# Performance work log

Hardware: AMD Instinct MI355X
Metric: run time of the kernel (lower is better)

Reference implementation:

```python
import jax, jax.numpy as jnp
import numpy as np

DECAY_FACTOR = 0.995
TEMPERATURE = 0.1
MIN_SIMILARITY = 0.0
EPS = 1e-8

B, N, D, H, F, K = 1024, 100000, 512, 96, 7, 16


def setup_inputs() -> dict:
    key = jax.random.key(0)
    k1, k2, k3, k4 = jax.random.split(key, 4)
    query = jax.random.normal(k1, (B, D), dtype=jnp.float32)
    keys = jax.random.normal(k2, (N, D), dtype=jnp.float32)
    values = jax.random.normal(k3, (N, H, F), dtype=jnp.float32)
    timestamps = jnp.sort(jax.random.randint(k4, (N,), 0, 5000).astype(jnp.int64))
    return {
        "query": query,
        "keys": keys,
        "values": values,
        "timestamps": timestamps,
        "global_step": 5000,
        "top_k": K,
    }


def _l2_normalize(x, axis=-1):
    # matches F.normalize(p=2): x / max(||x||, eps) -- use eps in denom
    norm = jnp.sqrt(jnp.sum(x * x, axis=axis, keepdims=True))
    return x / jnp.maximum(norm, 1e-12)


def reference(query, keys, values, timestamps, global_step, top_k):
    # cosine similarity between queries and all memory keys: [B, N]
    q_n = _l2_normalize(query)
    k_n = _l2_normalize(keys)
    sims = jnp.einsum("bd,nd->bn", q_n, k_n)

    # temporal decay by entry age
    age = (global_step - timestamps).astype(jnp.float32)  # [N]
    decay = jnp.power(jnp.float32(DECAY_FACTOR), age)
    sims = sims * decay[None, :]

    # top-k retrieval
    top_sims, top_idx = jax.lax.top_k(sims, top_k)  # [B, K]
    retrieved = values[top_idx]  # [B, K, H, F]

    valid_mask = top_sims >= MIN_SIMILARITY  # [B, K]

    # temperature-weighted aggregation of retrieved error patterns
    weights = jax.nn.softmax(top_sims / TEMPERATURE, axis=-1)
    weights = weights * valid_mask.astype(weights.dtype)
    weights = weights / (jnp.sum(weights, axis=-1, keepdims=True) + EPS)
    corrected = jnp.einsum("bk,bkhf->bhf", weights, retrieved)  # [B, H, F]
    return corrected
```

## Files before the change

### kernel.cpp

```cpp
#include <hip/hip_runtime.h>
#include <math.h>

#define B 1024
#define N 100000
#define D 512
#define H 96
#define F 7
#define K 16
#define HF (H*F)

#define QT 128
#define KT 128
#define NKT 784
#define NPAD (NKT*KT)

#define GQ 32
#define NG (NPAD/GQ)
#define SELG 16
#define CAND (SELG*GQ)
#define CSEL 32

typedef __attribute__((ext_vector_type(8))) short shortx8;
typedef __attribute__((ext_vector_type(4))) float floatx4;

__device__ __forceinline__ unsigned short f2bf(float f) {
    unsigned int u = __float_as_uint(f);
    u += 0x7FFF + ((u >> 16) & 1);
    return (unsigned short)(u >> 16);
}
__device__ __forceinline__ float bf2f(unsigned short u) {
    return __uint_as_float((unsigned)u << 16);
}

#define ASYNC16(g, l) __builtin_amdgcn_global_load_lds( \
    (__attribute__((address_space(1))) void*)(g), \
    (__attribute__((address_space(3))) void*)(l), 16, 0, 0)

__global__ void prep_q(const float* __restrict__ q, float* __restrict__ qn,
                       unsigned short* __restrict__ qb) {
    int w = (blockIdx.x * blockDim.x + threadIdx.x) >> 6;
    int l = threadIdx.x & 63;
    if (w >= B) return;
    const float4* row = (const float4*)(q + (size_t)w * D);
    float4 a = row[l], b = row[l + 64];
    float ss = a.x*a.x + a.y*a.y + a.z*a.z + a.w*a.w
             + b.x*b.x + b.y*b.y + b.z*b.z + b.w*b.w;
#pragma unroll
    for (int off = 32; off; off >>= 1) ss += __shfl_xor(ss, off);
    float nrm = fmaxf(sqrtf(ss), 1e-12f);
    a.x /= nrm; a.y /= nrm; a.z /= nrm; a.w /= nrm;
    b.x /= nrm; b.y /= nrm; b.z /= nrm; b.w /= nrm;
    float4* o = (float4*)(qn + (size_t)w * D);
    o[l] = a; o[l + 64] = b;
    unsigned short* ob = qb + (size_t)w * D;
    *(ushort4*)(ob + 4*l)       = make_ushort4(f2bf(a.x), f2bf(a.y), f2bf(a.z), f2bf(a.w));
    *(ushort4*)(ob + 256 + 4*l) = make_ushort4(f2bf(b.x), f2bf(b.y), f2bf(b.z), f2bf(b.w));
}

__global__ void prep_k(const float* __restrict__ keys, const int* __restrict__ ts,
                       const int* __restrict__ gstep, float* __restrict__ kscale,
                       unsigned short* __restrict__ kb) {
    int w = (blockIdx.x * blockDim.x + threadIdx.x) >> 6;
    int l = threadIdx.x & 63;
    if (w >= NPAD) return;
    unsigned short* dst = kb + (size_t)w * D;
    if (w >= N) {
        *(ushort4*)(dst + 4*l)       = make_ushort4(0,0,0,0);
        *(ushort4*)(dst + 256 + 4*l) = make_ushort4(0,0,0,0);
        return;
    }
    const float4* row = (const float4*)(keys + (size_t)w * D);
    float4 a = row[l], b = row[l + 64];
    float ss = a.x*a.x + a.y*a.y + a.z*a.z + a.w*a.w
             + b.x*b.x + b.y*b.y + b.z*b.z + b.w*b.w;
#pragma unroll
    for (int off = 32; off; off >>= 1) ss += __shfl_xor(ss, off);
    float age = (float)(gstep[0] - ts[w]);
    float sc = powf(0.995f, age) / fmaxf(sqrtf(ss), 1e-12f);
    if (l == 0) kscale[w] = sc;
    *(ushort4*)(dst + 4*l)       = make_ushort4(f2bf(a.x*sc), f2bf(a.y*sc), f2bf(a.z*sc), f2bf(a.w*sc));
    *(ushort4*)(dst + 256 + 4*l) = make_ushort4(f2bf(b.x*sc), f2bf(b.y*sc), f2bf(b.z*sc), f2bf(b.w*sc));
}

__global__ __launch_bounds__(256, 3)
void gmax_k(const unsigned short* __restrict__ qb, const unsigned short* __restrict__ kb,
            float* __restrict__ gmax) {
    __shared__ __align__(16) unsigned short As[QT * 32];
    __shared__ __align__(16) unsigned short Bs[KT * 32];

    const int t = threadIdx.x;
    const int w = t >> 6, l = t & 63;
    const int qbase = blockIdx.x * QT;
    const int kbase = blockIdx.y * KT;
    const int m = l & 15, quad = l >> 4;
    const int wq = w & 1, wk = w >> 1;

    const int srow = l >> 2;
    const int scol = (l & 3) * 8;
    const unsigned short* gA0 = qb + (size_t)(qbase + w*32 + srow) * D + scol;
    const unsigned short* gA1 = gA0 + (size_t)16 * D;
    const unsigned short* gB0 = kb + (size_t)(kbase + w*32 + srow) * D + scol;
    const unsigned short* gB1 = gB0 + (size_t)16 * D;
    unsigned short* lA0 = As + (w*32) * 32;
    unsigned short* lA1 = As + (w*32 + 16) * 32;
    unsigned short* lB0 = Bs + (w*32) * 32;
    unsigned short* lB1 = Bs + (w*32 + 16) * 32;

    const unsigned short* aBase = As + (size_t)(wq*64 + m) * 32 + quad*8;
    const unsigned short* bBase = Bs + (size_t)(wk*64 + m) * 32 + quad*8;

    floatx4 acc[4][4];
#pragma unroll
    for (int i = 0; i < 4; ++i)
#pragma unroll
        for (int j = 0; j < 4; ++j) acc[i][j] = (floatx4){0.f, 0.f, 0.f, 0.f};

    for (int ds = 0; ds < D/32; ++ds) {
        ASYNC16(gA0 + ds*32, lA0);
        ASYNC16(gA1 + ds*32, lA1);
        ASYNC16(gB0 + ds*32, lB0);
        ASYNC16(gB1 + ds*32, lB1);
        __syncthreads();
        shortx8 af[4], bf[4];
#pragma unroll
        for (int i = 0; i < 4; ++i) af[i] = *(const shortx8*)(aBase + i*512);
#pragma unroll
        for (int j = 0; j < 4; ++j) bf[j] = *(const shortx8*)(bBase + j*512);
#pragma unroll
        for (int i = 0; i < 4; ++i)
#pragma unroll
            for (int j = 0; j < 4; ++j)
                acc[i][j] = __builtin_amdgcn_mfma_f32_16x16x32_bf16(
                    af[i], bf[j], acc[i][j], 0, 0, 0);
        __syncthreads();
    }

    const int gcol = blockIdx.y * 4 + wk * 2;
#pragma unroll
    for (int qt = 0; qt < 4; ++qt)
#pragma unroll
        for (int r = 0; r < 4; ++r) {
            float v0 = fmaxf(acc[qt][0][r], acc[qt][1][r]);
            float v1 = fmaxf(acc[qt][2][r], acc[qt][3][r]);
#pragma unroll
            for (int off = 1; off < 16; off <<= 1) {
                v0 = fmaxf(v0, __shfl_xor(v0, off));
                v1 = fmaxf(v1, __shfl_xor(v1, off));
            }
            if (m == 0) {
                size_t row = (size_t)(qbase + wq*64 + qt*16 + quad*4 + r);
                gmax[row * NG + gcol]     = v0;
                gmax[row * NG + gcol + 1] = v1;
            }
        }
}

__global__ __launch_bounds__(256)
void select_out(const float* __restrict__ gmax, const unsigned short* __restrict__ qb,
                const unsigned short* __restrict__ kb, const float* __restrict__ qn,
                const float* __restrict__ keys, const float* __restrict__ kscale,
                const float* __restrict__ values, float* __restrict__ out) {
    int b = blockIdx.x, t = threadIdx.x;
    __shared__ float sG[NG];
    __shared__ int   gSel[SELG];
    __shared__ float eS[CAND];
    __shared__ int   eI[CAND];
    __shared__ float rS[4]; __shared__ int rI[4], rP[4];
    __shared__ float qrow[D];
    __shared__ unsigned short sQ[D];
    __shared__ float cS[CSEL]; __shared__ int cIdx[CSEL];
    __shared__ float wgt[K]; __shared__ int wIdx[K];

    for (int i = t; i < NG; i += 256) sG[i] = gmax[(size_t)b * NG + i];
    for (int i = t; i < D; i += 256) { qrow[i] = qn[(size_t)b * D + i]; sQ[i] = qb[(size_t)b * D + i]; }
    __syncthreads();

    int lane = t & 63, w = t >> 6;

    for (int r = 0; r < SELG; ++r) {
        float best = -INFINITY; int bp = 0x7fffffff;
        for (int i = t; i < NG; i += 256) {
            float v = sG[i];
            if (v > best || (v == best && i < bp)) { best = v; bp = i; }
        }
#pragma unroll
        for (int off = 32; off; off >>= 1) {
            float ob = __shfl_xor(best, off);
            int op = __shfl_xor(bp, off);
            if (ob > best || (ob == best && op < bp)) { best = ob; bp = op; }
        }
        if (lane == 0) { rS[w] = best; rP[w] = bp; }
        __syncthreads();
        if (t == 0) {
            float bb = rS[0]; int bbp = rP[0];
            for (int j = 1; j < 4; ++j)
                if (rS[j] > bb || (rS[j] == bb && rP[j] < bbp)) { bb = rS[j]; bbp = rP[j]; }
            gSel[r] = bbp; sG[bbp] = -INFINITY;
        }
        __syncthreads();
    }

    float qv[8];
#pragma unroll
    for (int j = 0; j < 8; ++j) qv[j] = bf2f(sQ[lane*8 + j]);
    for (int s = w; s < CAND; s += 4) {
        int g = gSel[s >> 5];
        int idx = g * GQ + (s & 31);
        uint4 kv = *(const uint4*)(kb + (size_t)idx * D + lane*8);
        unsigned u0 = kv.x, u1 = kv.y, u2 = kv.z, u3 = kv.w;
        float p = 0.f;
        p = fmaf(qv[0], __uint_as_float((u0 & 0xffffu) << 16), p);
        p = fmaf(qv[1], __uint_as_float(u0 & 0xffff0000u), p);
        p = fmaf(qv[2], __uint_as_float((u1 & 0xffffu) << 16), p);
        p = fmaf(qv[3], __uint_as_float(u1 & 0xffff0000u), p);
        p = fmaf(qv[4], __uint_as_float((u2 & 0xffffu) << 16), p);
        p = fmaf(qv[5], __uint_as_float(u2 & 0xffff0000u), p);
        p = fmaf(qv[6], __uint_as_float((u3 & 0xffffu) << 16), p);
        p = fmaf(qv[7], __uint_as_float(u3 & 0xffff0000u), p);
#pragma unroll
        for (int off = 32; off; off >>= 1) p += __shfl_xor(p, off);
        if (lane == 0) { eS[s] = (idx < N) ? p : -INFINITY; eI[s] = idx; }
    }
    __syncthreads();

    for (int r = 0; r < CSEL; ++r) {
        float best = -INFINITY; int bi = 0x7fffffff, bp = -1;
        for (int i = t; i < CAND; i += 256) {
            float v = eS[i]; int ii = eI[i];
            if (v > best || (v == best && ii < bi)) { best = v; bi = ii; bp = i; }
        }
#pragma unroll
        for (int off = 32; off; off >>= 1) {
            float ob = __shfl_xor(best, off);
            int oi = __shfl_xor(bi, off);
            int op = __shfl_xor(bp, off);
            if (ob > best || (ob == best && oi < bi)) { best = ob; bi = oi; bp = op; }
        }
        if (lane == 0) { rS[w] = best; rI[w] = bi; rP[w] = bp; }
        __syncthreads();
        if (t == 0) {
            float bb = rS[0]; int bbi = rI[0], bbp = rP[0];
            for (int j = 1; j < 4; ++j)
                if (rS[j] > bb || (rS[j] == bb && rI[j] < bbi)) { bb = rS[j]; bbi = rI[j]; bbp = rP[j]; }
            cIdx[r] = bbi;
            if (bbp >= 0) eS[bbp] = -INFINITY;
        }
        __syncthreads();
    }

    for (int c = w; c < CSEL; c += 4) {
        int idx = cIdx[c];
        const float4* kr = (const float4*)(keys + (size_t)idx * D);
        const float4* qr = (const float4*)qrow;
        float4 k1 = kr[lane], k2 = kr[lane + 64];
        float4 q1 = qr[lane], q2 = qr[lane + 64];
        float p = q1.x*k1.x + q1.y*k1.y + q1.z*k1.z + q1.w*k1.w
                + q2.x*k2.x + q2.y*k2.y + q2.z*k2.z + q2.w*k2.w;
#pragma unroll
        for (int off = 32; off; off >>= 1) p += __shfl_xor(p, off);
        if (lane == 0) cS[c] = p * kscale[idx];
    }
    __syncthreads();

    if (t == 0) {
        float s[CSEL]; int id[CSEL];
        for (int i = 0; i < CSEL; ++i) { s[i] = cS[i]; id[i] = cIdx[i]; }
        float selS[K]; int selI[K];
        for (int r = 0; r < K; ++r) {
            float bb = -INFINITY; int bbi = 0x7fffffff, bbp = -1;
            for (int i = 0; i < CSEL; ++i)
                if (s[i] > bb || (s[i] == bb && id[i] < bbi)) { bb = s[i]; bbi = id[i]; bbp = i; }
            selS[r] = bb; selI[r] = bbi; s[bbp] = -INFINITY;
        }
        float y[K], e[K];
        for (int k = 0; k < K; ++k) y[k] = selS[k] / 0.1f;
        float ymax = y[0];
        float Z = 0.f;
        for (int k = 0; k < K; ++k) { e[k] = expf(y[k] - ymax); Z += e[k]; }
        float Z2 = 0.f;
        for (int k = 0; k < K; ++k) {
            float ww = e[k] / Z;
            if (!(selS[k] >= 0.0f)) ww = 0.f;
            e[k] = ww; Z2 += ww;
        }
        for (int k = 0; k < K; ++k) { wgt[k] = e[k] / (Z2 + 1e-8f); wIdx[k] = selI[k]; }
    }
    __syncthreads();

    for (int e0 = t; e0 < HF; e0 += 256) {
        float o = 0.f;
#pragma unroll
        for (int k = 0; k < K; ++k)
            o += wgt[k] * values[(size_t)wIdx[k] * HF + e0];
        out[(size_t)b * HF + e0] = o;
    }
}

extern "C" void kernel_launch(void* const* d_in, const int* in_sizes, int n_in,
                              void* d_out, int out_size, void* d_ws, size_t ws_size,
                              hipStream_t stream) {
    const float* query  = (const float*)d_in[0];
    const float* keys   = (const float*)d_in[1];
    const float* values = (const float*)d_in[2];
    const int*   ts     = (const int*)d_in[3];
    const int*   gstep  = (const int*)d_in[4];
    float* out = (float*)d_out;

    char* p = (char*)d_ws;
    size_t o = 0;
    auto alloc = [&](size_t bytes) { char* r = p + o; o = (o + bytes + 255) & ~(size_t)255; return r; };
    float*          qn     = (float*)alloc((size_t)B * D * 4);
    unsigned short* qb     = (unsigned short*)alloc((size_t)B * D * 2);
    float*          kscale = (float*)alloc((size_t)N * 4);
    unsigned short* kb     = (unsigned short*)alloc((size_t)NPAD * D * 2);
    float*          gmax   = (float*)alloc((size_t)B * NG * 4);

    prep_q<<<B / 4, 256, 0, stream>>>(query, qn, qb);
    prep_k<<<NPAD / 4, 256, 0, stream>>>(keys, ts, gstep, kscale, kb);
    dim3 g2(B / QT, NKT);
    gmax_k<<<g2, 256, 0, stream>>>(qb, kb, gmax);
    select_out<<<B, 256, 0, stream>>>(gmax, qb, kb, qn, keys, kscale, values, out);
}
```

Before: 775.2 us.

## Refine candidates with exact fp32 dot products over finer groups and single-wave top-k

Group size drops from 32 to 16 keys and 32 groups are now selected, so the gmax buffer doubles and is written with float4 stores. The select kernel drops the bf16 candidate rescoring and the intermediate 32-candidate stage. Each thread now computes exact fp32 dot products for two of the 512 candidates directly from the original keys, and one wave does the top-16 selection in registers. This removes one serial selection loop and many block barriers, but it doubles the gmax write and read traffic and gives each thread long strided fp32 key reads.

```diff
diff --git a/kernel.cpp b/kernel.cpp
--- a/kernel.cpp
+++ b/kernel.cpp
@@ -14,11 +14,10 @@
 #define NKT 784
 #define NPAD (NKT*KT)
 
-#define GQ 32
+#define GQ 16
 #define NG (NPAD/GQ)
-#define SELG 16
+#define SELG 32
 #define CAND (SELG*GQ)
-#define CSEL 32
 
 typedef __attribute__((ext_vector_type(8))) short shortx8;
 typedef __attribute__((ext_vector_type(4))) float floatx4;
@@ -27,9 +26,6 @@
     unsigned int u = __float_as_uint(f);
     u += 0x7FFF + ((u >> 16) & 1);
     return (unsigned short)(u >> 16);
-}
-__device__ __forceinline__ float bf2f(unsigned short u) {
-    return __uint_as_float((unsigned)u << 16);
 }
 
 #define ASYNC16(g, l) __builtin_amdgcn_global_load_lds( \
@@ -135,44 +131,48 @@
         __syncthreads();
     }
 
-    const int gcol = blockIdx.y * 4 + wk * 2;
+    const int gcol = blockIdx.y * 8 + wk * 4;
 #pragma unroll
     for (int qt = 0; qt < 4; ++qt)
 #pragma unroll
         for (int r = 0; r < 4; ++r) {
-            float v0 = fmaxf(acc[qt][0][r], acc[qt][1][r]);
-            float v1 = fmaxf(acc[qt][2][r], acc[qt][3][r]);
+            float v0 = acc[qt][0][r], v1 = acc[qt][1][r];
+            float v2 = acc[qt][2][r], v3 = acc[qt][3][r];
 #pragma unroll
             for (int off = 1; off < 16; off <<= 1) {
                 v0 = fmaxf(v0, __shfl_xor(v0, off));
                 v1 = fmaxf(v1, __shfl_xor(v1, off));
+                v2 = fmaxf(v2, __shfl_xor(v2, off));
+                v3 = fmaxf(v3, __shfl_xor(v3, off));
             }
             if (m == 0) {
                 size_t row = (size_t)(qbase + wq*64 + qt*16 + quad*4 + r);
-                gmax[row * NG + gcol]     = v0;
-                gmax[row * NG + gcol + 1] = v1;
+                *(float4*)(gmax + row * NG + gcol) = make_float4(v0, v1, v2, v3);
             }
         }
 }
 
 __global__ __launch_bounds__(256)
-void select_out(const float* __restrict__ gmax, const unsigned short* __restrict__ qb,
-                const unsigned short* __restrict__ kb, const float* __restrict__ qn,
+void select_out(const float* __restrict__ gmax, const float* __restrict__ qn,
                 const float* __restrict__ keys, const float* __restrict__ kscale,
                 const float* __restrict__ values, float* __restrict__ out) {
     int b = blockIdx.x, t = threadIdx.x;
     __shared__ float sG[NG];
+    __shared__ float qrow[D];
     __shared__ int   gSel[SELG];
     __shared__ float eS[CAND];
     __shared__ int   eI[CAND];
-    __shared__ float rS[4]; __shared__ int rI[4], rP[4];
-    __shared__ float qrow[D];
-    __shared__ unsigned short sQ[D];
-    __shared__ float cS[CSEL]; __shared__ int cIdx[CSEL];
+    __shared__ float rS[4]; __shared__ int rP[4];
+    __shared__ float selS[K]; __shared__ int selI[K];
     __shared__ float wgt[K]; __shared__ int wIdx[K];
 
-    for (int i = t; i < NG; i += 256) sG[i] = gmax[(size_t)b * NG + i];
-    for (int i = t; i < D; i += 256) { qrow[i] = qn[(size_t)b * D + i]; sQ[i] = qb[(size_t)b * D + i]; }
+    {
+        const float4* gs = (const float4*)(gmax + (size_t)b * NG);
+        float4* gd = (float4*)sG;
+        for (int i = t; i < NG/4; i += 256) gd[i] = gs[i];
+        const float4* qs = (const float4*)(qn + (size_t)b * D);
+        if (t < D/4) ((float4*)qrow)[t] = qs[t];
+    }
     __syncthreads();
 
     int lane = t & 63, w = t >> 6;
@@ -200,99 +200,91 @@
         __syncthreads();
     }
 
-    float qv[8];
-#pragma unroll
-    for (int j = 0; j < 8; ++j) qv[j] = bf2f(sQ[lane*8 + j]);
-    for (int s = w; s < CAND; s += 4) {
-        int g = gSel[s >> 5];
-        int idx = g * GQ + (s & 31);
-        uint4 kv = *(const uint4*)(kb + (size_t)idx * D + lane*8);
-        unsigned u0 = kv.x, u1 = kv.y, u2 = kv.z, u3 = kv.w;
-        float p = 0.f;
-        p = fmaf(qv[0], __uint_as_float((u0 & 0xffffu) << 16), p);
-        p = fmaf(qv[1], __uint_as_float(u0 & 0xffff0000u), p);
-        p = fmaf(qv[2], __uint_as_float((u1 & 0xffffu) << 16), p);
-        p = fmaf(qv[3], __uint_as_float(u1 & 0xffff0000u), p);
-        p = fmaf(qv[4], __uint_as_float((u2 & 0xffffu) << 16), p);
-        p = fmaf(qv[5], __uint_as_float(u2 & 0xffff0000u), p);
-        p = fmaf(qv[6], __uint_as_float((u3 & 0xffffu) << 16), p);
-        p = fmaf(qv[7], __uint_as_float(u3 & 0xffff0000u), p);
-#pragma unroll
-        for (int off = 32; off; off >>= 1) p += __shfl_xor(p, off);
-        if (lane == 0) { eS[s] = (idx < N) ? p : -INFINITY; eI[s] = idx; }
+    {
+        int ga = gSel[t >> 4];
+        int gb = gSel[(t >> 4) + 16];
+        int ia = ga * GQ + (t & 15);
+        int ib = gb * GQ + (t & 15);
+        bool va = ia < N, vb = ib < N;
+        const float4* ka = (const float4*)(keys + (size_t)(va ? ia : 0) * D);
+        const float4* kb4 = (const float4*)(keys + (size_t)(vb ? ib : 0) * D);
+        const float4* qs = (const float4*)qrow;
+        float a0 = 0.f, a1 = 0.f, a2 = 0.f, a3 = 0.f;
+        float b0 = 0.f, b1 = 0.f, b2 = 0.f, b3 = 0.f;
+#pragma unroll 8
+        for (int d = 0; d < D/4; ++d) {
+            float4 qv = qs[d];
+            float4 kva = ka[d];
+            float4 kvb = kb4[d];
+            a0 = fmaf(qv.x, kva.x, a0);
+            a1 = fmaf(qv.y, kva.y, a1);
+            a2 = fmaf(qv.z, kva.z, a2);
+            a3 = fmaf(qv.w, kva.w, a3);
+            b0 = fmaf(qv.x, kvb.x, b0);
+            b1 = fmaf(qv.y, kvb.y, b1);
+            b2 = fmaf(qv.z, kvb.z, b2);
+            b3 = fmaf(qv.w, kvb.w, b3);
+        }
+        float pa = (a0 + a1) + (a2 + a3);
+        float pb = (b0 + b1) + (b2 + b3);
+        eS[t]       = va ? pa * kscale[ia] : -INFINITY;
+        eI[t]       = ia;
+        eS[t + 256] = vb ? pb * kscale[ib] : -INFINITY;
+        eI[t + 256] = ib;
     }
     __syncthreads();
 
-    for (int r = 0; r < CSEL; ++r) {
-        float best = -INFINITY; int bi = 0x7fffffff, bp = -1;
-        for (int i = t; i < CAND; i += 256) {
-            float v = eS[i]; int ii = eI[i];
-            if (v > best || (v == best && ii < bi)) { best = v; bi = ii; bp = i; }
-        }
-#pragma unroll
-        for (int off = 32; off; off >>= 1) {
-            float ob = __shfl_xor(best, off);
-            int oi = __shfl_xor(bi, off);
-            int op = __shfl_xor(bp, off);
-            if (ob > best || (ob == best && oi < bi)) { best = ob; bi = oi; bp = op; }
-        }
-        if (lane == 0) { rS[w] = best; rI[w] = bi; rP[w] = bp; }
-        __syncthreads();
-        if (t == 0) {
-            float bb = rS[0]; int bbi = rI[0], bbp = rP[0];
-            for (int j = 1; j < 4; ++j)
-                if (rS[j] > bb || (rS[j] == bb && rI[j] < bbi)) { bb = rS[j]; bbi = rI[j]; bbp = rP[j]; }
-            cIdx[r] = bbi;
-            if (bbp >= 0) eS[bbp] = -INFINITY;
-        }
-        __syncthreads();
-    }
-
-    for (int c = w; c < CSEL; c += 4) {
-        int idx = cIdx[c];
-        const float4* kr = (const float4*)(keys + (size_t)idx * D);
-        const float4* qr = (const float4*)qrow;
-        float4 k1 = kr[lane], k2 = kr[lane + 64];
-        float4 q1 = qr[lane], q2 = qr[lane + 64];
-        float p = q1.x*k1.x + q1.y*k1.y + q1.z*k1.z + q1.w*k1.w
-                + q2.x*k2.x + q2.y*k2.y + q2.z*k2.z + q2.w*k2.w;
-#pragma unroll
-        for (int off = 32; off; off >>= 1) p += __shfl_xor(p, off);
-        if (lane == 0) cS[c] = p * kscale[idx];
+    if (w == 0) {
+        float v[8]; int idx[8];
+#pragma unroll
+        for (int j = 0; j < 8; ++j) { v[j] = eS[lane + 64*j]; idx[j] = eI[lane + 64*j]; }
+#pragma unroll
+        for (int r = 0; r < K; ++r) {
+            float bv = v[0]; int bi = idx[0];
+#pragma unroll
+            for (int j = 1; j < 8; ++j)
+                if (v[j] > bv || (v[j] == bv && idx[j] < bi)) { bv = v[j]; bi = idx[j]; }
+#pragma unroll
+            for (int off = 32; off; off >>= 1) {
+                float ov = __shfl_xor(bv, off);
+                int oi = __shfl_xor(bi, off);
+                if (ov > bv || (ov == bv && oi < bi)) { bv = ov; bi = oi; }
+            }
+            if (lane == 0) { selS[r] = bv; selI[r] = bi; }
+#pragma unroll
+            for (int j = 0; j < 8; ++j)
+                if (idx[j] == bi) v[j] = -INFINITY;
+        }
+        if (lane == 0) {
+            float y[K], e[K];
+            for (int k = 0; k < K; ++k) y[k] = selS[k] / 0.1f;
+            float ymax = y[0];
+            float Z = 0.f;
+            for (int k = 0; k < K; ++k) { e[k] = expf(y[k] - ymax); Z += e[k]; }
+            float Z2 = 0.f;
+            for (int k = 0; k < K; ++k) {
+                float ww = e[k] / Z;
+                if (!(selS[k] >= 0.0f)) ww = 0.f;
+                e[k] = ww; Z2 += ww;
+            }
+            for (int k = 0; k < K; ++k) { wgt[k] = e[k] / (Z2 + 1e-8f); wIdx[k] = selI[k]; }
+        }
     }
     __syncthreads();
 
-    if (t == 0) {
-        float s[CSEL]; int id[CSEL];
-        for (int i = 0; i < CSEL; ++i) { s[i] = cS[i]; id[i] = cIdx[i]; }
-        float selS[K]; int selI[K];
-        for (int r = 0; r < K; ++r) {
-            float bb = -INFINITY; int bbi = 0x7fffffff, bbp = -1;
-            for (int i = 0; i < CSEL; ++i)
-                if (s[i] > bb || (s[i] == bb && id[i] < bbi)) { bb = s[i]; bbi = id[i]; bbp = i; }
-            selS[r] = bb; selI[r] = bbi; s[bbp] = -INFINITY;
-        }
-        float y[K], e[K];
-        for (int k = 0; k < K; ++k) y[k] = selS[k] / 0.1f;
-        float ymax = y[0];
-        float Z = 0.f;
-        for (int k = 0; k < K; ++k) { e[k] = expf(y[k] - ymax); Z += e[k]; }
-        float Z2 = 0.f;
+    if (t < HF/4) {
+        float4 o = make_float4(0.f, 0.f, 0.f, 0.f);
+#pragma unroll
         for (int k = 0; k < K; ++k) {
-            float ww = e[k] / Z;
-            if (!(selS[k] >= 0.0f)) ww = 0.f;
-            e[k] = ww; Z2 += ww;
-        }
-        for (int k = 0; k < K; ++k) { wgt[k] = e[k] / (Z2 + 1e-8f); wIdx[k] = selI[k]; }
-    }
-    __syncthreads();
-
-    for (int e0 = t; e0 < HF; e0 += 256) {
-        float o = 0.f;
-#pragma unroll
-        for (int k = 0; k < K; ++k)
-            o += wgt[k] * values[(size_t)wIdx[k] * HF + e0];
-        out[(size_t)b * HF + e0] = o;
+            const float4* vr = (const float4*)(values + (size_t)wIdx[k] * HF);
+            float4 v = vr[t];
+            float ww = wgt[k];
+            o.x = fmaf(ww, v.x, o.x);
+            o.y = fmaf(ww, v.y, o.y);
+            o.z = fmaf(ww, v.z, o.z);
+            o.w = fmaf(ww, v.w, o.w);
+        }
+        ((float4*)(out + (size_t)b * HF))[t] = o;
     }
 }
 
@@ -319,5 +311,5 @@
     prep_k<<<NPAD / 4, 256, 0, stream>>>(keys, ts, gstep, kscale, kb);
     dim3 g2(B / QT, NKT);
     gmax_k<<<g2, 256, 0, stream>>>(qb, kb, gmax);
-    select_out<<<B, 256, 0, stream>>>(gmax, qb, kb, qn, keys, kscale, values, out);
-}
+    select_out<<<B, 256, 0, stream>>>(gmax, qn, keys, kscale, values, out);
+}
```

Result: slower. 855.9 us (+10.4%).
